# Optimization experiments

Measured on AMD Instinct MI355X. Metric: run time of the kernel, lower is better.

The kernel has to match this reference:

```python
import jax, jax.numpy as jnp
import numpy as np

KSIZE = 13
BETA = 0.97
THR = 1.0
SMIN, SMAX = 0.4, 10.0


def gaussian_kernel(sigma):
    # matches torch: coarse grid [-6,6] (13 pts), normalized by sum over fine grid [-60,60] (130 pts)
    r = jnp.linspace(-(KSIZE // 2), KSIZE // 2, KSIZE)
    r_all = jnp.linspace(-(KSIZE // 2) * 10.0, (KSIZE // 2) * 10.0, KSIZE * 10)
    k = jnp.exp(-0.5 * (r / sigma) ** 2)
    norm = jnp.sum(jnp.exp(-0.5 * (r_all / sigma) ** 2))
    return k / norm


def setup_inputs() -> dict:
    key = jax.random.key(0)
    k1, = jax.random.split(key, 1)
    B, C, T = 512, 224, 224
    inp = jax.random.normal(k1, (B, 1, C, T), dtype=jnp.float32)
    w = jnp.float32((SMIN + SMAX) / 2.0)  # 5.2, init value of nn.Parameter
    return {"inp": inp, "w": w}


def reference(inp, w):
    x = inp[:, 0]                      # (B, C, T)
    B, C, T = x.shape
    wc = jnp.clip(w, SMIN, SMAX)
    kern = gaussian_kernel(wc)          # (K,), symmetric
    pad = (KSIZE - 1) // 2

    # gaussian smoothing across the channel axis, same kernel for every t and b
    # x_mean[b,c,t] = sum_k kern[k] * pad_C(x)[b, c+k, t]
    xc = x.transpose(0, 2, 1).reshape(B * T, 1, C)   # (B*T, 1, C)
    xm = jax.lax.conv_general_dilated(
        xc, kern.reshape(1, 1, KSIZE),
        window_strides=(1,), padding=[(pad, pad)],
        dimension_numbers=("NCH", "OIH", "NCH"))
    x_mean = xm.reshape(B, T, C).transpose(0, 2, 1)  # (B, C, T)

    # input current: clip x at the smoothed mean from above
    I = x - jax.nn.relu(x - x_mean)                   # (B, C, T)

    # snn.Leaky (beta=0.97, threshold=1, reset_mechanism='subtract')
    def step(mem, I_t):
        reset = (mem > THR).astype(mem.dtype)         # reset based on previous mem
        mem = BETA * mem + I_t - reset * THR
        spk = (mem > THR).astype(mem.dtype)           # Heaviside(mem - threshold)
        return mem, spk

    mem0 = jnp.zeros((B, C), x.dtype)
    _, spk = jax.lax.scan(step, mem0, I.transpose(2, 0, 1))  # (T, B, C)
    spk = spk.transpose(1, 2, 0)[:, None]                    # (B, 1, C, T)
    return spk
```

## Files before the change

kernel.cpp:

```cpp
#include <hip/hip_runtime.h>

constexpr int Cc   = 224;
constexpr int Tt   = 224;
constexpr int TT   = 32;
constexpr int NT   = Tt / TT;
constexpr int LDW  = 36;
constexpr int ROWS = 236;
constexpr int BUFW = ROWS * LDW;
constexpr int BDIM = 256;

__global__ __launch_bounds__(BDIM, 2)
void cgss_snn_kernel(const float* __restrict__ x,
                     const float* __restrict__ wp,
                     float* __restrict__ out)
{
    __shared__ float lds[2 * BUFW];

    const int tid = threadIdx.x;
    const int w   = tid >> 6;
    const int l   = tid & 63;
    const long long bofs = (long long)blockIdx.x * (Cc * Tt);
    const float* xb = x + bofs;
    float*       ob = out + bofs;

    if (tid < 192) {
        int bufi = tid / 96;
        int q    = tid - 96 * bufi;
        int rr   = q >> 3;
        int slot = q & 7;
        int row  = (rr < 6) ? rr : (224 + rr);
        *reinterpret_cast<float4*>(&lds[bufi * BUFW + row * LDW + slot * 4]) =
            make_float4(0.f, 0.f, 0.f, 0.f);
    }

    const int srow = l >> 3;
    const int stq  = l & 7;
    const int rowbase = 56 * w + srow;

    float4 vst[7];
#pragma unroll
    for (int i = 0; i < 7; ++i)
        vst[i] = *reinterpret_cast<const float4*>(
            xb + (rowbase + 8 * i) * Tt + 4 * stq);

    float kr[13];
    {
        float wv = wp[0];
        float wc = fminf(fmaxf(wv, 0.4f), 10.0f);
        float norm = 0.0f;
        const float step = 120.0f / 129.0f;
        for (int j = 0; j < 130; ++j) {
            float r = -60.0f + (float)j * step;
            float z = r / wc;
            norm += expf(-0.5f * z * z);
        }
        for (int i = 0; i < 13; ++i) {
            float r = (float)(i - 6);
            float z = r / wc;
            kr[i] = expf(-0.5f * z * z) / norm;
        }
    }

#pragma unroll
    for (int i = 0; i < 7; ++i)
        *reinterpret_cast<float4*>(
            &lds[(rowbase + 8 * i + 6) * LDW + 4 * stq]) = vst[i];
#pragma unroll
    for (int i = 0; i < 7; ++i)
        vst[i] = *reinterpret_cast<const float4*>(
            xb + (rowbase + 8 * i) * Tt + TT + 4 * stq);

    asm volatile("s_waitcnt lgkmcnt(0)" ::: "memory");
    __builtin_amdgcn_s_barrier();
    __builtin_amdgcn_sched_barrier(0);

    float mem = 0.f, rstv = 0.f;
    unsigned r0 = 0, r1 = 0, r2 = 0, r3 = 0, r4 = 0, r5 = 0, r6 = 0;
    int bufc = 0;

#pragma unroll 1
    for (int tile = 0; tile < NT; ++tile) {
        float* cur = &lds[bufc * BUFW];
        float* nxt = &lds[(bufc ^ 1) * BUFW];

        unsigned m = 0;
        if (tid < Cc) {
            const float* base = cur + tid * LDW;
#pragma unroll
            for (int tq = 0; tq < 8; ++tq) {
                float4 v[13];
#pragma unroll
                for (int k = 0; k < 13; ++k)
                    v[k] = *reinterpret_cast<const float4*>(base + k * LDW + 4 * tq);
                float4 acc = make_float4(0.f, 0.f, 0.f, 0.f);
#pragma unroll
                for (int k = 0; k < 13; ++k) {
                    float kk = kr[k];
                    acc.x += kk * v[k].x;  acc.y += kk * v[k].y;
                    acc.z += kk * v[k].z;  acc.w += kk * v[k].w;
                }
                const float* xv = (const float*)&v[6];
                const float* av = (const float*)&acc;
#pragma unroll
                for (int s = 0; s < 4; ++s) {
                    float d  = xv[s] - av[s];
                    float rl = d > 0.0f ? d : 0.0f;
                    float I  = xv[s] - rl;
                    mem = 0.97f * mem + I - rstv;
                    bool sp = mem > 1.0f;
                    rstv = sp ? 1.0f : 0.0f;
                    m |= sp ? (1u << (4 * tq + s)) : 0u;
                }
            }
        }
        r0 = r1; r1 = r2; r2 = r3; r3 = r4; r4 = r5; r5 = r6; r6 = m;

        if (tile < NT - 1) {
#pragma unroll
            for (int i = 0; i < 7; ++i)
                *reinterpret_cast<float4*>(
                    &nxt[(rowbase + 8 * i + 6) * LDW + 4 * stq]) = vst[i];
        }
        if (tile < NT - 2) {
            const float* src = xb + (tile + 2) * TT + 4 * stq;
#pragma unroll
            for (int i = 0; i < 7; ++i)
                vst[i] = *reinterpret_cast<const float4*>(
                    src + (rowbase + 8 * i) * Tt);
        }

        if (tile < NT - 1) {
            asm volatile("s_waitcnt lgkmcnt(0)" ::: "memory");
            __builtin_amdgcn_s_barrier();
            __builtin_amdgcn_sched_barrier(0);
        }
        bufc ^= 1;
    }

    unsigned* mw = reinterpret_cast<unsigned*>(&lds[BUFW]);
    if (tid < Cc) {
        const int mb = tid * 9;
        mw[mb + 0] = r0; mw[mb + 1] = r1; mw[mb + 2] = r2; mw[mb + 3] = r3;
        mw[mb + 4] = r4; mw[mb + 5] = r5; mw[mb + 6] = r6;
    }
    asm volatile("s_waitcnt lgkmcnt(0)" ::: "memory");
    __builtin_amdgcn_s_barrier();
    __builtin_amdgcn_sched_barrier(0);

#pragma unroll 1
    for (int i = 0; i < 7; ++i) {
        const int cr = rowbase + 8 * i;
        float* dst = ob + (long long)cr * Tt + 4 * stq;
        const unsigned* mrow = mw + cr * 9;
#pragma unroll
        for (int k = 0; k < 7; ++k) {
            unsigned mk = mrow[k];
            unsigned rb = mk >> (4 * stq);
            float4 s4;
            s4.x = (rb & 1u) ? 1.0f : 0.0f;
            s4.y = (rb & 2u) ? 1.0f : 0.0f;
            s4.z = (rb & 4u) ? 1.0f : 0.0f;
            s4.w = (rb & 8u) ? 1.0f : 0.0f;
            *reinterpret_cast<float4*>(dst + k * TT) = s4;
        }
    }
}

extern "C" void kernel_launch(void* const* d_in, const int* in_sizes, int n_in,
                              void* d_out, int out_size, void* d_ws, size_t ws_size,
                              hipStream_t stream)
{
    const float* x  = (const float*)d_in[0];
    const float* w  = (const float*)d_in[1];
    float* out      = (float*)d_out;
    const int B = in_sizes[0] / (Cc * Tt);
    cgss_snn_kernel<<<B, BDIM, 0, stream>>>(x, w, out);
}
```

Measured before the change: 83.80 us.

## Stream spike output stores during the tile loop instead of at the end

Spike masks used to be kept in registers and all written to global memory after the scan finished. Now, every two tiles, the masks are staged in LDS and all threads write 64-column chunks of output (256-byte rows), which overlaps the output stores with later compute. The last tile is written in the epilogue. This adds one barrier in the final iteration plus extra LDS traffic, and relies on the barrier ordering mask writes and reads across iterations.

```diff
diff --git a/kernel.cpp b/kernel.cpp
--- a/kernel.cpp
+++ b/kernel.cpp
@@ -8,13 +8,17 @@
 constexpr int ROWS = 236;
 constexpr int BUFW = ROWS * LDW;
 constexpr int BDIM = 256;
+constexpr int MSKOFF  = 2 * BUFW;
+constexpr int TAILOFF = 2 * BUFW + 512;
 
 __global__ __launch_bounds__(BDIM, 2)
 void cgss_snn_kernel(const float* __restrict__ x,
                      const float* __restrict__ wp,
                      float* __restrict__ out)
 {
-    __shared__ float lds[2 * BUFW];
+    __shared__ float lds[2 * BUFW + 512 + 256];
+    unsigned* msk  = reinterpret_cast<unsigned*>(&lds[MSKOFF]);
+    unsigned* tmsk = reinterpret_cast<unsigned*>(&lds[TAILOFF]);
 
     const int tid = threadIdx.x;
     const int w   = tid >> 6;
@@ -36,6 +40,10 @@
     const int srow = l >> 3;
     const int stq  = l & 7;
     const int rowbase = 56 * w + srow;
+    const int r2 = l >> 4;
+    const int o  = l & 15;
+    const int osel = o >> 3;
+    const int osh  = (o & 7) * 4;
 
     float4 vst[7];
 #pragma unroll
@@ -75,7 +83,7 @@
     __builtin_amdgcn_sched_barrier(0);
 
     float mem = 0.f, rstv = 0.f;
-    unsigned r0 = 0, r1 = 0, r2 = 0, r3 = 0, r4 = 0, r5 = 0, r6 = 0;
+    unsigned mprev = 0;
     int bufc = 0;
 
 #pragma unroll 1
@@ -113,7 +121,14 @@
                 }
             }
         }
-        r0 = r1; r1 = r2; r2 = r3; r3 = r4; r4 = r5; r5 = r6; r6 = m;
+
+        if (tile & 1) {
+            msk[2 * tid]     = mprev;
+            msk[2 * tid + 1] = m;
+        } else {
+            mprev = m;
+        }
+        if (tile == NT - 1) tmsk[tid] = m;
 
         if (tile < NT - 1) {
 #pragma unroll
@@ -129,40 +144,40 @@
                     src + (rowbase + 8 * i) * Tt);
         }
 
-        if (tile < NT - 1) {
-            asm volatile("s_waitcnt lgkmcnt(0)" ::: "memory");
-            __builtin_amdgcn_s_barrier();
-            __builtin_amdgcn_sched_barrier(0);
+        asm volatile("s_waitcnt lgkmcnt(0)" ::: "memory");
+        __builtin_amdgcn_s_barrier();
+        __builtin_amdgcn_sched_barrier(0);
+
+        if (tile & 1) {
+            const int p = tile >> 1;
+#pragma unroll
+            for (int j = 0; j < 14; ++j) {
+                int cr = 56 * w + 4 * j + r2;
+                unsigned mk = msk[2 * cr + osel];
+                unsigned rb = mk >> osh;
+                float4 s4;
+                s4.x = (rb & 1u) ? 1.0f : 0.0f;
+                s4.y = (rb & 2u) ? 1.0f : 0.0f;
+                s4.z = (rb & 4u) ? 1.0f : 0.0f;
+                s4.w = (rb & 8u) ? 1.0f : 0.0f;
+                *reinterpret_cast<float4*>(
+                    &ob[(long long)cr * Tt + 64 * p + 4 * o]) = s4;
+            }
         }
         bufc ^= 1;
     }
 
-    unsigned* mw = reinterpret_cast<unsigned*>(&lds[BUFW]);
-    if (tid < Cc) {
-        const int mb = tid * 9;
-        mw[mb + 0] = r0; mw[mb + 1] = r1; mw[mb + 2] = r2; mw[mb + 3] = r3;
-        mw[mb + 4] = r4; mw[mb + 5] = r5; mw[mb + 6] = r6;
-    }
-    asm volatile("s_waitcnt lgkmcnt(0)" ::: "memory");
-    __builtin_amdgcn_s_barrier();
-    __builtin_amdgcn_sched_barrier(0);
-
-#pragma unroll 1
+#pragma unroll
     for (int i = 0; i < 7; ++i) {
-        const int cr = rowbase + 8 * i;
-        float* dst = ob + (long long)cr * Tt + 4 * stq;
-        const unsigned* mrow = mw + cr * 9;
-#pragma unroll
-        for (int k = 0; k < 7; ++k) {
-            unsigned mk = mrow[k];
-            unsigned rb = mk >> (4 * stq);
-            float4 s4;
-            s4.x = (rb & 1u) ? 1.0f : 0.0f;
-            s4.y = (rb & 2u) ? 1.0f : 0.0f;
-            s4.z = (rb & 4u) ? 1.0f : 0.0f;
-            s4.w = (rb & 8u) ? 1.0f : 0.0f;
-            *reinterpret_cast<float4*>(dst + k * TT) = s4;
-        }
+        int cr = rowbase + 8 * i;
+        unsigned mk = tmsk[cr];
+        unsigned rb = mk >> (4 * stq);
+        float4 s4;
+        s4.x = (rb & 1u) ? 1.0f : 0.0f;
+        s4.y = (rb & 2u) ? 1.0f : 0.0f;
+        s4.z = (rb & 4u) ? 1.0f : 0.0f;
+        s4.w = (rb & 8u) ? 1.0f : 0.0f;
+        *reinterpret_cast<float4*>(&ob[(long long)cr * Tt + 192 + 4 * stq]) = s4;
     }
 }
 
```

Result: no change. 83.88 us (+0.1%).
